# Optimization experiments

Hardware: AMD Instinct MI355X
Metric: run time of the kernel (lower is better)

## Reference

```python
import jax, jax.numpy as jnp
import numpy as np

N_NODES = 100000
N_EDGES = 1600000
EMB = 128
EDGE_F = 16
BN_EPS = 1e-5


def _gin_conv(x, src, dst, edge_attr, w1, b1, bn_w, bn_b, w2, b2, ew, eb):
    # edge embedding: F.linear(edge_attr, edge_w, edge_b) -> [E, d]
    edge_emb = edge_attr @ ew.T + eb
    n = x.shape[0]
    # scatter-add aggregation of messages concat(x_j, edge_emb) at dst.
    # Self loops contribute (x_i, linear(0)=eb); add them analytically instead
    # of materializing the augmented edge list (same math as add_self_loops).
    agg_x = jax.ops.segment_sum(x[src], dst, num_segments=n) + x
    agg_e = jax.ops.segment_sum(edge_emb, dst, num_segments=n) + eb
    h = jnp.concatenate([agg_x, agg_e], axis=1)          # [N, 2d]
    h = h @ w1.T + b1                                     # [N, 2d]
    # batch norm with training=True -> batch statistics (biased variance)
    mean = jnp.mean(h, axis=0)
    var = jnp.mean((h - mean) ** 2, axis=0)
    h = (h - mean) * jax.lax.rsqrt(var + BN_EPS) * bn_w + bn_b
    h = jax.nn.relu(h)
    return h @ w2.T + b2                                  # [N, d]


def setup_inputs() -> dict:
    key = jax.random.key(0)
    ks = jax.random.split(key, 12)
    s = 0.05
    x = jax.random.normal(ks[0], (N_NODES, EMB), jnp.float32)
    edge_attr = jax.random.uniform(ks[1], (N_EDGES, EDGE_F), jnp.float32)
    edge_index = jax.random.randint(ks[2], (2, N_EDGES), 0, N_NODES, jnp.int32)
    W1 = jax.random.normal(ks[3], (5, 2 * EMB, 2 * EMB), jnp.float32) * s
    B1 = jax.random.normal(ks[4], (5, 2 * EMB), jnp.float32) * s
    BNW = jax.random.uniform(ks[5], (5, 2 * EMB), jnp.float32, 0.5, 1.5)
    BNB = jax.random.normal(ks[6], (5, 2 * EMB), jnp.float32) * s
    W2 = jax.random.normal(ks[7], (5, EMB, 2 * EMB), jnp.float32) * s
    B2 = jax.random.normal(ks[8], (5, EMB), jnp.float32) * s
    EW = jax.random.normal(ks[9], (5, EMB, EDGE_F), jnp.float32) * s
    EB = jax.random.normal(ks[10], (5, EMB), jnp.float32) * s
    return {"x": x, "edge_attr": edge_attr, "W1": W1, "B1": B1, "BNW": BNW,
            "BNB": BNB, "W2": W2, "B2": B2, "EW": EW, "EB": EB,
            "edge_index": edge_index}


def reference(x, edge_attr, W1, B1, BNW, BNB, W2, B2, EW, EB, edge_index):
    src, dst = edge_index[0], edge_index[1]
    h = x
    for l in range(5):  # 5 structurally distinct layers (fixed small count)
        h = _gin_conv(h, src, dst, edge_attr, W1[l], B1[l], BNW[l], BNB[l],
                      W2[l], B2[l], EW[l], EB[l])
        if l < 4:
            h = jax.nn.relu(h)
        # dropout with drop_ratio=0 is identity
    return h
```

## Files before the change

### kernel.cpp

```cpp
#include <hip/hip_runtime.h>
#include <hip/hip_bf16.h>

#define N_NODES 100000
#define N_EDGES 1600000
#define EMB 128
#define D2 256
#define EDGE_F 16
#define BN_EPS 1e-5f
#define BK 64
#define SK 72
#define NSCB 98

typedef __hip_bfloat16 bf16;
typedef __attribute__((ext_vector_type(8))) short bf16x8;
typedef __attribute__((ext_vector_type(4))) float f32x4;

__device__ __forceinline__ bf16 f2b(float v) { return __float2bfloat16(v); }
__device__ __forceinline__ unsigned short f2bu(float v) {
    bf16 b = __float2bfloat16(v);
    return *(unsigned short*)&b;
}

__device__ int   g_deg[N_NODES];
__device__ int   g_rowoff[N_NODES + 1];
__device__ int   g_cur[N_NODES];
__device__ int   g_csr[N_EDGES];
__device__ int   g_blksum[NSCB];
__device__ int   g_blkoff[NSCB];
__device__ float g_agg[N_NODES * EDGE_F];
__device__ float g_bnacc[2 * D2];
__device__ float g_bncoef[2 * D2];
__device__ bf16  g_t[(size_t)N_NODES * D2];
__device__ float g_h1[(size_t)N_NODES * D2];
__device__ float g_xbuf[(size_t)N_NODES * EMB];
__device__ bf16  g_w1b[D2 * D2];
__device__ bf16  g_w2b[EMB * D2];


__global__ void k_init() {
    int i = blockIdx.x * blockDim.x + threadIdx.x;
    int stride = gridDim.x * blockDim.x;
    for (int j = i; j < N_NODES; j += stride) g_deg[j] = 0;
    for (int j = i; j < N_NODES * EDGE_F; j += stride) g_agg[j] = 0.f;
}

__global__ void k_edge(const int* __restrict__ ei, const float* __restrict__ ea) {
    int idx = blockIdx.x * blockDim.x + threadIdx.x;
    if (idx >= N_EDGES * EDGE_F) return;
    int e = idx >> 4;
    int f = idx & 15;
    int d = ei[N_EDGES + e];
    if (f == 0) atomicAdd(&g_deg[d], 1);
    atomicAdd(&g_agg[d * EDGE_F + f], ea[idx]);
}

__global__ void k_scan1() {
    __shared__ int s[1024];
    int tid = threadIdx.x;
    int i = blockIdx.x * 1024 + tid;
    int v = (i < N_NODES) ? g_deg[i] : 0;
    s[tid] = v;
    __syncthreads();
    for (int off = 1; off < 1024; off <<= 1) {
        int v2 = s[tid];
        if (tid >= off) v2 += s[tid - off];
        __syncthreads();
        s[tid] = v2;
        __syncthreads();
    }
    if (i < N_NODES) g_rowoff[i + 1] = s[tid];
    if (tid == 1023) g_blksum[blockIdx.x] = s[1023];
}

__global__ void k_scan2() {
    __shared__ int s[128];
    int tid = threadIdx.x;
    int v = (tid < NSCB) ? g_blksum[tid] : 0;
    s[tid] = v;
    __syncthreads();
    for (int off = 1; off < 128; off <<= 1) {
        int v2 = s[tid];
        if (tid >= off) v2 += s[tid - off];
        __syncthreads();
        s[tid] = v2;
        __syncthreads();
    }
    if (tid < NSCB) g_blkoff[tid] = s[tid] - v;
}

__global__ void k_scan3() {
    int i = blockIdx.x * blockDim.x + threadIdx.x;
    if (i == 0) g_rowoff[0] = 0;
    if (i < N_NODES) {
        int r = g_rowoff[i + 1] + g_blkoff[i >> 10];
        g_rowoff[i + 1] = r;
        g_cur[i] = r - g_deg[i];
    }
}

__global__ void k_fill(const int* __restrict__ ei) {
    int e = blockIdx.x * blockDim.x + threadIdx.x;
    if (e >= N_EDGES) return;
    int d = ei[N_EDGES + e];
    int pos = atomicAdd(&g_cur[d], 1);
    g_csr[pos] = ei[e];
}

__global__ void k_cvt(const float* __restrict__ W1l, const float* __restrict__ W2l) {
    int i = blockIdx.x * blockDim.x + threadIdx.x;
    if (i < D2 * D2) g_w1b[i] = f2b(W1l[i]);
    int j = i - D2 * D2;
    if (j >= 0 && j < EMB * D2) g_w2b[j] = f2b(W2l[j]);
}


template <bool FIRST>
__global__ __launch_bounds__(256) void k_agg(const float* __restrict__ x0,
                                             const float* __restrict__ EWl,
                                             const float* __restrict__ EBl) {
    int tid = threadIdx.x;
    if (blockIdx.x == 0) {
        g_bnacc[tid] = 0.f;
        g_bnacc[tid + 256] = 0.f;
    }
    int g = tid >> 5, lane32 = tid & 31;
    int v = blockIdx.x * 8 + g;
    __shared__ float sa[8][EDGE_F];
    if (lane32 < EDGE_F) sa[g][lane32] = g_agg[v * EDGE_F + lane32];
    __syncthreads();

    const float* src = FIRST ? x0 : g_xbuf;
    int r0 = g_rowoff[v], r1 = g_rowoff[v + 1];
    int deg = r1 - r0;
    float4 acc = *(const float4*)&src[(size_t)v * EMB + lane32 * 4];

    for (int base = r0; base < r1; base += 32) {
        int nb = r1 - base;
        if (nb > 32) nb = 32;
        int idx = (lane32 < nb) ? g_csr[base + lane32] : 0;
        int j = 0;
        for (; j + 4 <= nb; j += 4) {
            int u0 = __shfl(idx, j, 32);
            int u1 = __shfl(idx, j + 1, 32);
            int u2 = __shfl(idx, j + 2, 32);
            int u3 = __shfl(idx, j + 3, 32);
            float4 a0 = *(const float4*)&src[(size_t)u0 * EMB + lane32 * 4];
            float4 a1 = *(const float4*)&src[(size_t)u1 * EMB + lane32 * 4];
            float4 a2 = *(const float4*)&src[(size_t)u2 * EMB + lane32 * 4];
            float4 a3 = *(const float4*)&src[(size_t)u3 * EMB + lane32 * 4];
            acc.x += (a0.x + a1.x) + (a2.x + a3.x);
            acc.y += (a0.y + a1.y) + (a2.y + a3.y);
            acc.z += (a0.z + a1.z) + (a2.z + a3.z);
            acc.w += (a0.w + a1.w) + (a2.w + a3.w);
        }
        for (; j < nb; ++j) {
            int u = __shfl(idx, j, 32);
            float4 a0 = *(const float4*)&src[(size_t)u * EMB + lane32 * 4];
            acc.x += a0.x; acc.y += a0.y; acc.z += a0.z; acc.w += a0.w;
        }
    }
    ushort4 o;
    o.x = f2bu(acc.x); o.y = f2bu(acc.y); o.z = f2bu(acc.z); o.w = f2bu(acc.w);
    *(ushort4*)&g_t[(size_t)v * D2 + lane32 * 4] = o;

    float dp1 = (float)(deg + 1);
    ushort4 o2;
    unsigned short* op = (unsigned short*)&o2;
#pragma unroll
    for (int cc = 0; cc < 4; ++cc) {
        int f = lane32 * 4 + cc;
        float s2 = 0.f;
#pragma unroll
        for (int k = 0; k < EDGE_F; ++k) s2 += sa[g][k] * EWl[f * EDGE_F + k];
        s2 += dp1 * EBl[f];
        op[cc] = f2bu(s2);
    }
    *(ushort4*)&g_t[(size_t)v * D2 + EMB + lane32 * 4] = o2;
}

__global__ __launch_bounds__(256) void k_gemm1(const float* __restrict__ B1l) {
    __shared__ __align__(16) short sA[128 * SK];
    __shared__ __align__(16) short sB[128 * SK];
    int tid = threadIdx.x;
    int r0 = blockIdx.x * 128;
    int c0 = blockIdx.y * 128;
    int w = tid >> 6, lane = tid & 63;
    int wr = (w >> 1) * 64, wc = (w & 1) * 64;
    int ln = lane & 15, lq = lane >> 4;
    f32x4 acc[4][4] = {};
    const uint4* gt = (const uint4*)g_t;
    const uint4* gw = (const uint4*)g_w1b;
    for (int kk = 0; kk < D2; kk += BK) {
#pragma unroll
        for (int t = 0; t < 4; ++t) {
            int idx = tid + t * 256;
            int row = idx >> 3, seg = idx & 7;
            int r = r0 + row;
            uint4 val = make_uint4(0, 0, 0, 0);
            if (r < N_NODES) val = gt[(size_t)r * 32 + (kk >> 3) + seg];
            *(uint4*)&sA[row * SK + seg * 8] = val;
        }
#pragma unroll
        for (int t = 0; t < 4; ++t) {
            int idx = tid + t * 256;
            int row = idx >> 3, seg = idx & 7;
            *(uint4*)&sB[row * SK + seg * 8] = gw[(size_t)(c0 + row) * 32 + (kk >> 3) + seg];
        }
        __syncthreads();
#pragma unroll
        for (int k0 = 0; k0 < BK; k0 += 32) {
            bf16x8 af[4], bg[4];
#pragma unroll
            for (int a = 0; a < 4; ++a)
                af[a] = *(const bf16x8*)&sA[(wr + a * 16 + ln) * SK + k0 + lq * 8];
#pragma unroll
            for (int b = 0; b < 4; ++b)
                bg[b] = *(const bf16x8*)&sB[(wc + b * 16 + ln) * SK + k0 + lq * 8];
#pragma unroll
            for (int a = 0; a < 4; ++a)
#pragma unroll
                for (int b = 0; b < 4; ++b)
                    acc[a][b] = __builtin_amdgcn_mfma_f32_16x16x32_bf16(af[a], bg[b],
                                                                        acc[a][b], 0, 0, 0);
        }
        __syncthreads();
    }
    float sacc[4] = {0.f, 0.f, 0.f, 0.f};
    float qacc[4] = {0.f, 0.f, 0.f, 0.f};
#pragma unroll
    for (int a = 0; a < 4; ++a) {
#pragma unroll
        for (int r = 0; r < 4; ++r) {
            int row = r0 + wr + a * 16 + lq * 4 + r;
            if (row < N_NODES) {
#pragma unroll
                for (int b = 0; b < 4; ++b) {
                    int col = c0 + wc + b * 16 + ln;
                    float h = acc[a][b][r] + B1l[col];
                    g_h1[(size_t)row * D2 + col] = h;
                    sacc[b] += h;
                    qacc[b] += h * h;
                }
            }
        }
    }
#pragma unroll
    for (int b = 0; b < 4; ++b) {
        float s = sacc[b], q = qacc[b];
        s += __shfl_xor(s, 16); q += __shfl_xor(q, 16);
        s += __shfl_xor(s, 32); q += __shfl_xor(q, 32);
        if (lq == 0) {
            int col = c0 + wc + b * 16 + ln;
            atomicAdd(&g_bnacc[col], s);
            atomicAdd(&g_bnacc[D2 + col], q);
        }
    }
}

__global__ void k_bnfin(const float* __restrict__ BNWl, const float* __restrict__ BNBl) {
    int c = threadIdx.x;
    float inv_n = 1.f / (float)N_NODES;
    float mean = g_bnacc[c] * inv_n;
    float var = g_bnacc[D2 + c] * inv_n - mean * mean;
    float sc = BNWl[c] * rsqrtf(var + BN_EPS);
    g_bncoef[c] = sc;
    g_bncoef[D2 + c] = BNBl[c] - mean * sc;
}

template <bool LAST>
__global__ __launch_bounds__(256) void k_gemm2(const float* __restrict__ B2l,
                                               float* __restrict__ out) {
    __shared__ __align__(16) short sA[128 * SK];
    __shared__ __align__(16) short sB[128 * SK];
    __shared__ __align__(16) float sC[2 * D2];
    int tid = threadIdx.x;
    sC[tid] = g_bncoef[tid];
    sC[tid + 256] = g_bncoef[tid + 256];
    __syncthreads();
    int r0 = blockIdx.x * 128;
    int w = tid >> 6, lane = tid & 63;
    int wr = (w >> 1) * 64, wc = (w & 1) * 64;
    int ln = lane & 15, lq = lane >> 4;
    f32x4 acc[4][4] = {};
    const uint4* gw = (const uint4*)g_w2b;
    for (int kk = 0; kk < D2; kk += BK) {
#pragma unroll
        for (int t = 0; t < 8; ++t) {
            int idx = tid + t * 256;
            int row = idx >> 4, seg = idx & 15;
            int r = r0 + row;
            int k = kk + seg * 4;
            ushort4 o = make_ushort4(0, 0, 0, 0);
            if (r < N_NODES) {
                float4 v = *(const float4*)&g_h1[(size_t)r * D2 + k];
                float4 s = *(const float4*)&sC[k];
                float4 h = *(const float4*)&sC[D2 + k];
                o.x = f2bu(fmaxf(v.x * s.x + h.x, 0.f));
                o.y = f2bu(fmaxf(v.y * s.y + h.y, 0.f));
                o.z = f2bu(fmaxf(v.z * s.z + h.z, 0.f));
                o.w = f2bu(fmaxf(v.w * s.w + h.w, 0.f));
            }
            *(ushort4*)&sA[row * SK + seg * 4] = o;
        }
#pragma unroll
        for (int t = 0; t < 4; ++t) {
            int idx = tid + t * 256;
            int row = idx >> 3, seg = idx & 7;
            *(uint4*)&sB[row * SK + seg * 8] = gw[(size_t)row * 32 + (kk >> 3) + seg];
        }
        __syncthreads();
#pragma unroll
        for (int k0 = 0; k0 < BK; k0 += 32) {
            bf16x8 af[4], bg[4];
#pragma unroll
            for (int a = 0; a < 4; ++a)
                af[a] = *(const bf16x8*)&sA[(wr + a * 16 + ln) * SK + k0 + lq * 8];
#pragma unroll
            for (int b = 0; b < 4; ++b)
                bg[b] = *(const bf16x8*)&sB[(wc + b * 16 + ln) * SK + k0 + lq * 8];
#pragma unroll
            for (int a = 0; a < 4; ++a)
#pragma unroll
                for (int b = 0; b < 4; ++b)
                    acc[a][b] = __builtin_amdgcn_mfma_f32_16x16x32_bf16(af[a], bg[b],
                                                                        acc[a][b], 0, 0, 0);
        }
        __syncthreads();
    }
#pragma unroll
    for (int a = 0; a < 4; ++a) {
#pragma unroll
        for (int r = 0; r < 4; ++r) {
            int row = r0 + wr + a * 16 + lq * 4 + r;
            if (row < N_NODES) {
#pragma unroll
                for (int b = 0; b < 4; ++b) {
                    int col = wc + b * 16 + ln;
                    float v = acc[a][b][r] + B2l[col];
                    if (LAST) out[(size_t)row * EMB + col] = v;
                    else      g_xbuf[(size_t)row * EMB + col] = fmaxf(v, 0.f);
                }
            }
        }
    }
}

extern "C" void kernel_launch(void* const* d_in, const int* in_sizes, int n_in,
                              void* d_out, int out_size, void* d_ws, size_t ws_size,
                              hipStream_t stream) {
    const float* x0 = (const float*)d_in[0];
    const float* ea = (const float*)d_in[1];
    const float* W1 = (const float*)d_in[2];
    const float* B1 = (const float*)d_in[3];
    const float* BNW = (const float*)d_in[4];
    const float* BNB = (const float*)d_in[5];
    const float* W2 = (const float*)d_in[6];
    const float* B2 = (const float*)d_in[7];
    const float* EW = (const float*)d_in[8];
    const float* EB = (const float*)d_in[9];
    const int* ei = (const int*)d_in[10];

    k_init<<<4096, 256, 0, stream>>>();
    k_edge<<<(N_EDGES * EDGE_F + 255) / 256, 256, 0, stream>>>(ei, ea);
    k_scan1<<<NSCB, 1024, 0, stream>>>();
    k_scan2<<<1, 128, 0, stream>>>();
    k_scan3<<<(N_NODES + 255) / 256, 256, 0, stream>>>();
    k_fill<<<(N_EDGES + 255) / 256, 256, 0, stream>>>(ei);

    const int GB = (N_NODES + 127) / 128;
    for (int l = 0; l < 5; ++l) {
        const float* W1l = W1 + (size_t)l * D2 * D2;
        const float* B1l = B1 + (size_t)l * D2;
        const float* BNWl = BNW + (size_t)l * D2;
        const float* BNBl = BNB + (size_t)l * D2;
        const float* W2l = W2 + (size_t)l * EMB * D2;
        const float* B2l = B2 + (size_t)l * EMB;
        const float* EWl = EW + (size_t)l * EMB * EDGE_F;
        const float* EBl = EB + (size_t)l * EMB;

        k_cvt<<<(D2 * D2 + EMB * D2 + 255) / 256, 256, 0, stream>>>(W1l, W2l);

        if (l == 0)
            k_agg<true><<<N_NODES / 8, 256, 0, stream>>>(x0, EWl, EBl);
        else
            k_agg<false><<<N_NODES / 8, 256, 0, stream>>>(nullptr, EWl, EBl);

        k_gemm1<<<dim3(GB, 2), 256, 0, stream>>>(B1l);
        k_bnfin<<<1, 256, 0, stream>>>(BNWl, BNBl);

        if (l < 4)
            k_gemm2<false><<<dim3(GB, 1), 256, 0, stream>>>(B2l, nullptr);
        else
            k_gemm2<true><<<dim3(GB, 1), 256, 0, stream>>>(B2l, (float*)d_out);
    }
}
```

Before: 1.955 ms.

## Store node features in bf16 for gather, batch weight conversion, fuse BN finalize

```diff
diff --git a/kernel.cpp b/kernel.cpp
--- a/kernel.cpp
+++ b/kernel.cpp
@@ -20,6 +20,12 @@
     bf16 b = __float2bfloat16(v);
     return *(unsigned short*)&b;
 }
+__device__ __forceinline__ float bs2f(short s) {
+    unsigned int u = ((unsigned int)(unsigned short)s) << 16;
+    float f;
+    __builtin_memcpy(&f, &u, 4);
+    return f;
+}
 
 __device__ int   g_deg[N_NODES];
 __device__ int   g_rowoff[N_NODES + 1];
@@ -29,12 +35,11 @@
 __device__ int   g_blkoff[NSCB];
 __device__ float g_agg[N_NODES * EDGE_F];
 __device__ float g_bnacc[2 * D2];
-__device__ float g_bncoef[2 * D2];
+__device__ bf16  g_xb[(size_t)N_NODES * EMB];
 __device__ bf16  g_t[(size_t)N_NODES * D2];
 __device__ float g_h1[(size_t)N_NODES * D2];
-__device__ float g_xbuf[(size_t)N_NODES * EMB];
-__device__ bf16  g_w1b[D2 * D2];
-__device__ bf16  g_w2b[EMB * D2];
+__device__ bf16  g_w1b[5 * D2 * D2];
+__device__ bf16  g_w2b[5 * EMB * D2];
 
 
 __global__ void k_init() {
@@ -42,6 +47,15 @@
     int stride = gridDim.x * blockDim.x;
     for (int j = i; j < N_NODES; j += stride) g_deg[j] = 0;
     for (int j = i; j < N_NODES * EDGE_F; j += stride) g_agg[j] = 0.f;
+}
+
+__global__ void k_prep(const float* __restrict__ x0, const float* __restrict__ W1,
+                       const float* __restrict__ W2) {
+    int i0 = blockIdx.x * blockDim.x + threadIdx.x;
+    int st = gridDim.x * blockDim.x;
+    for (int i = i0; i < 5 * D2 * D2; i += st) g_w1b[i] = f2b(W1[i]);
+    for (int i = i0; i < 5 * EMB * D2; i += st) g_w2b[i] = f2b(W2[i]);
+    for (int i = i0; i < N_NODES * EMB; i += st) g_xb[i] = f2b(x0[i]);
 }
 
 __global__ void k_edge(const int* __restrict__ ei, const float* __restrict__ ea) {
@@ -106,79 +120,72 @@
     g_csr[pos] = ei[e];
 }
 
-__global__ void k_cvt(const float* __restrict__ W1l, const float* __restrict__ W2l) {
-    int i = blockIdx.x * blockDim.x + threadIdx.x;
-    if (i < D2 * D2) g_w1b[i] = f2b(W1l[i]);
-    int j = i - D2 * D2;
-    if (j >= 0 && j < EMB * D2) g_w2b[j] = f2b(W2l[j]);
-}
-
-
-template <bool FIRST>
-__global__ __launch_bounds__(256) void k_agg(const float* __restrict__ x0,
-                                             const float* __restrict__ EWl,
+
+__global__ __launch_bounds__(256) void k_agg(const float* __restrict__ EWl,
                                              const float* __restrict__ EBl) {
     int tid = threadIdx.x;
     if (blockIdx.x == 0) {
         g_bnacc[tid] = 0.f;
         g_bnacc[tid + 256] = 0.f;
     }
-    int g = tid >> 5, lane32 = tid & 31;
-    int v = blockIdx.x * 8 + g;
-    __shared__ float sa[8][EDGE_F];
-    if (lane32 < EDGE_F) sa[g][lane32] = g_agg[v * EDGE_F + lane32];
+    int g = tid >> 4, lane = tid & 15;
+    int v = blockIdx.x * 16 + g;
+    __shared__ float sa[16][17];
+    sa[g][lane] = g_agg[v * EDGE_F + lane];
     __syncthreads();
 
-    const float* src = FIRST ? x0 : g_xbuf;
+    const bf16x8* src = (const bf16x8*)g_xb;
+    float acc[8];
+    bf16x8 own = src[(size_t)v * 16 + lane];
+#pragma unroll
+    for (int i = 0; i < 8; ++i) acc[i] = bs2f(own[i]);
+
     int r0 = g_rowoff[v], r1 = g_rowoff[v + 1];
-    int deg = r1 - r0;
-    float4 acc = *(const float4*)&src[(size_t)v * EMB + lane32 * 4];
-
-    for (int base = r0; base < r1; base += 32) {
+    for (int base = r0; base < r1; base += 16) {
         int nb = r1 - base;
-        if (nb > 32) nb = 32;
-        int idx = (lane32 < nb) ? g_csr[base + lane32] : 0;
+        if (nb > 16) nb = 16;
+        int idx = (lane < nb) ? g_csr[base + lane] : 0;
         int j = 0;
         for (; j + 4 <= nb; j += 4) {
-            int u0 = __shfl(idx, j, 32);
-            int u1 = __shfl(idx, j + 1, 32);
-            int u2 = __shfl(idx, j + 2, 32);
-            int u3 = __shfl(idx, j + 3, 32);
-            float4 a0 = *(const float4*)&src[(size_t)u0 * EMB + lane32 * 4];
-            float4 a1 = *(const float4*)&src[(size_t)u1 * EMB + lane32 * 4];
-            float4 a2 = *(const float4*)&src[(size_t)u2 * EMB + lane32 * 4];
-            float4 a3 = *(const float4*)&src[(size_t)u3 * EMB + lane32 * 4];
-            acc.x += (a0.x + a1.x) + (a2.x + a3.x);
-            acc.y += (a0.y + a1.y) + (a2.y + a3.y);
-            acc.z += (a0.z + a1.z) + (a2.z + a3.z);
-            acc.w += (a0.w + a1.w) + (a2.w + a3.w);
+            int u0 = __shfl(idx, j, 16);
+            int u1 = __shfl(idx, j + 1, 16);
+            int u2 = __shfl(idx, j + 2, 16);
+            int u3 = __shfl(idx, j + 3, 16);
+            bf16x8 a0 = src[(size_t)u0 * 16 + lane];
+            bf16x8 a1 = src[(size_t)u1 * 16 + lane];
+            bf16x8 a2 = src[(size_t)u2 * 16 + lane];
+            bf16x8 a3 = src[(size_t)u3 * 16 + lane];
+#pragma unroll
+            for (int i = 0; i < 8; ++i)
+                acc[i] += (bs2f(a0[i]) + bs2f(a1[i])) + (bs2f(a2[i]) + bs2f(a3[i]));
         }
         for (; j < nb; ++j) {
-            int u = __shfl(idx, j, 32);
-            float4 a0 = *(const float4*)&src[(size_t)u * EMB + lane32 * 4];
-            acc.x += a0.x; acc.y += a0.y; acc.z += a0.z; acc.w += a0.w;
-        }
-    }
-    ushort4 o;
-    o.x = f2bu(acc.x); o.y = f2bu(acc.y); o.z = f2bu(acc.z); o.w = f2bu(acc.w);
-    *(ushort4*)&g_t[(size_t)v * D2 + lane32 * 4] = o;
-
-    float dp1 = (float)(deg + 1);
-    ushort4 o2;
-    unsigned short* op = (unsigned short*)&o2;
-#pragma unroll
-    for (int cc = 0; cc < 4; ++cc) {
-        int f = lane32 * 4 + cc;
+            int u = __shfl(idx, j, 16);
+            bf16x8 a0 = src[(size_t)u * 16 + lane];
+#pragma unroll
+            for (int i = 0; i < 8; ++i) acc[i] += bs2f(a0[i]);
+        }
+    }
+    bf16x8 ov;
+#pragma unroll
+    for (int i = 0; i < 8; ++i) ((unsigned short*)&ov)[i] = f2bu(acc[i]);
+    *(bf16x8*)&g_t[(size_t)v * D2 + lane * 8] = ov;
+
+    float dp1 = (float)(r1 - r0 + 1);
+    bf16x8 o2;
+#pragma unroll
+    for (int cc = 0; cc < 8; ++cc) {
+        int f = lane * 8 + cc;
         float s2 = 0.f;
 #pragma unroll
         for (int k = 0; k < EDGE_F; ++k) s2 += sa[g][k] * EWl[f * EDGE_F + k];
         s2 += dp1 * EBl[f];
-        op[cc] = f2bu(s2);
-    }
-    *(ushort4*)&g_t[(size_t)v * D2 + EMB + lane32 * 4] = o2;
-}
-
-__global__ __launch_bounds__(256) void k_gemm1(const float* __restrict__ B1l) {
+        ((unsigned short*)&o2)[cc] = f2bu(s2);
+    }
+    *(bf16x8*)&g_t[(size_t)v * D2 + EMB + lane * 8] = o2;
+}
+
+__global__ __launch_bounds__(256) void k_gemm1(const float* __restrict__ B1l, int l) {
     __shared__ __align__(16) short sA[128 * SK];
     __shared__ __align__(16) short sB[128 * SK];
     int tid = threadIdx.x;
@@ -189,7 +196,7 @@
     int ln = lane & 15, lq = lane >> 4;
     f32x4 acc[4][4] = {};
     const uint4* gt = (const uint4*)g_t;
-    const uint4* gw = (const uint4*)g_w1b;
+    const uint4* gw = (const uint4*)(g_w1b + (size_t)l * D2 * D2);
     for (int kk = 0; kk < D2; kk += BK) {
 #pragma unroll
         for (int t = 0; t < 4; ++t) {
@@ -257,32 +264,30 @@
     }
 }
 
-__global__ void k_bnfin(const float* __restrict__ BNWl, const float* __restrict__ BNBl) {
-    int c = threadIdx.x;
-    float inv_n = 1.f / (float)N_NODES;
-    float mean = g_bnacc[c] * inv_n;
-    float var = g_bnacc[D2 + c] * inv_n - mean * mean;
-    float sc = BNWl[c] * rsqrtf(var + BN_EPS);
-    g_bncoef[c] = sc;
-    g_bncoef[D2 + c] = BNBl[c] - mean * sc;
-}
-
 template <bool LAST>
-__global__ __launch_bounds__(256) void k_gemm2(const float* __restrict__ B2l,
+__global__ __launch_bounds__(256) void k_gemm2(const float* __restrict__ BNWl,
+                                               const float* __restrict__ BNBl,
+                                               const float* __restrict__ B2l, int l,
                                                float* __restrict__ out) {
     __shared__ __align__(16) short sA[128 * SK];
     __shared__ __align__(16) short sB[128 * SK];
     __shared__ __align__(16) float sC[2 * D2];
     int tid = threadIdx.x;
-    sC[tid] = g_bncoef[tid];
-    sC[tid + 256] = g_bncoef[tid + 256];
+    {
+        float inv_n = 1.f / (float)N_NODES;
+        float mean = g_bnacc[tid] * inv_n;
+        float var = g_bnacc[D2 + tid] * inv_n - mean * mean;
+        float scv = BNWl[tid] * rsqrtf(var + BN_EPS);
+        sC[tid] = scv;
+        sC[D2 + tid] = BNBl[tid] - mean * scv;
+    }
     __syncthreads();
     int r0 = blockIdx.x * 128;
     int w = tid >> 6, lane = tid & 63;
     int wr = (w >> 1) * 64, wc = (w & 1) * 64;
     int ln = lane & 15, lq = lane >> 4;
     f32x4 acc[4][4] = {};
-    const uint4* gw = (const uint4*)g_w2b;
+    const uint4* gw = (const uint4*)(g_w2b + (size_t)l * EMB * D2);
     for (int kk = 0; kk < D2; kk += BK) {
 #pragma unroll
         for (int t = 0; t < 8; ++t) {
@@ -338,7 +343,7 @@
                     int col = wc + b * 16 + ln;
                     float v = acc[a][b][r] + B2l[col];
                     if (LAST) out[(size_t)row * EMB + col] = v;
-                    else      g_xbuf[(size_t)row * EMB + col] = fmaxf(v, 0.f);
+                    else      g_xb[(size_t)row * EMB + col] = f2b(fmaxf(v, 0.f));
                 }
             }
         }
@@ -361,6 +366,7 @@
     const int* ei = (const int*)d_in[10];
 
     k_init<<<4096, 256, 0, stream>>>();
+    k_prep<<<2048, 256, 0, stream>>>(x0, W1, W2);
     k_edge<<<(N_EDGES * EDGE_F + 255) / 256, 256, 0, stream>>>(ei, ea);
     k_scan1<<<NSCB, 1024, 0, stream>>>();
     k_scan2<<<1, 128, 0, stream>>>();
@@ -369,28 +375,19 @@
 
     const int GB = (N_NODES + 127) / 128;
     for (int l = 0; l < 5; ++l) {
-        const float* W1l = W1 + (size_t)l * D2 * D2;
         const float* B1l = B1 + (size_t)l * D2;
         const float* BNWl = BNW + (size_t)l * D2;
         const float* BNBl = BNB + (size_t)l * D2;
-        const float* W2l = W2 + (size_t)l * EMB * D2;
         const float* B2l = B2 + (size_t)l * EMB;
         const float* EWl = EW + (size_t)l * EMB * EDGE_F;
         const float* EBl = EB + (size_t)l * EMB;
 
-        k_cvt<<<(D2 * D2 + EMB * D2 + 255) / 256, 256, 0, stream>>>(W1l, W2l);
-
-        if (l == 0)
-            k_agg<true><<<N_NODES / 8, 256, 0, stream>>>(x0, EWl, EBl);
+        k_agg<<<N_NODES / 16, 256, 0, stream>>>(EWl, EBl);
+        k_gemm1<<<dim3(GB, 2), 256, 0, stream>>>(B1l, l);
+        if (l < 4)
+            k_gemm2<false><<<dim3(GB, 1), 256, 0, stream>>>(BNWl, BNBl, B2l, l, nullptr);
         else
-            k_agg<false><<<N_NODES / 8, 256, 0, stream>>>(nullptr, EWl, EBl);
-
-        k_gemm1<<<dim3(GB, 2), 256, 0, stream>>>(B1l);
-        k_bnfin<<<1, 256, 0, stream>>>(BNWl, BNBl);
-
-        if (l < 4)
-            k_gemm2<false><<<dim3(GB, 1), 256, 0, stream>>>(B2l, nullptr);
-        else
-            k_gemm2<true><<<dim3(GB, 1), 256, 0, stream>>>(B2l, (float*)d_out);
-    }
-}
+            k_gemm2<true><<<dim3(GB, 1), 256, 0, stream>>>(BNWl, BNBl, B2l, l,
+                                                           (float*)d_out);
+    }
+}
```

Measured after the change: 2.242 ms. 1.15x slower.
